# Optimization experiments

Measured on AMD Instinct MI355X. Metric: run time of the kernel, lower is better.

Reference implementation:

```python
import jax, jax.numpy as jnp
import numpy as np

N = 100000      # nodes
E = 1600000     # edges (avg degree 16)
IN = 128        # in_channels
OUT = 64        # out_channels
HID = 2 * OUT   # hidden = 2*out_channels


def setup_inputs() -> dict:
    key = jax.random.key(0)
    ks = jax.random.split(key, 9)
    x = jax.random.normal(ks[0], (N, IN), jnp.float32)
    edge_index = jax.random.randint(ks[1], (2, E), 0, N, jnp.int32)
    init_dist = jax.random.normal(ks[2], (N, OUT), jnp.float32)
    # GCNConv weights (glorot-ish scale) and biases
    W1 = jax.random.normal(ks[3], (IN, HID), jnp.float32) * (1.0 / np.sqrt(IN))
    b1 = jnp.zeros((HID,), jnp.float32)
    Wmu = jax.random.normal(ks[4], (HID, OUT), jnp.float32) * (1.0 / np.sqrt(HID))
    bmu = jnp.zeros((OUT,), jnp.float32)
    Wls = jax.random.normal(ks[5], (HID, OUT), jnp.float32) * (1.0 / np.sqrt(HID))
    bls = jnp.zeros((OUT,), jnp.float32)
    return {"x": x, "edge_index": edge_index, "init_dist": init_dist,
            "W1": W1, "b1": b1, "Wmu": Wmu, "bmu": bmu, "Wls": Wls, "bls": bls}


def _gcn(h, src, dst, norm, W, b, n):
    # dense transform, then normalized scatter-add aggregation over edges
    h = h @ W                               # [N, F]
    msg = h[src] * norm[:, None]            # gather + scale  [E', F]
    out = jax.ops.segment_sum(msg, dst, num_segments=n)
    return out + b


def reference(x, edge_index, init_dist, W1, b1, Wmu, bmu, Wls, bls):
    n = x.shape[0]
    # add self-loops (PyG GCNConv default)
    loops = jnp.arange(n, dtype=edge_index.dtype)
    src = jnp.concatenate([edge_index[0], loops])
    dst = jnp.concatenate([edge_index[1], loops])
    # symmetric normalization: deg over A+I, norm_e = d_src^-1/2 * d_dst^-1/2
    deg = jax.ops.segment_sum(jnp.ones_like(dst, dtype=x.dtype), dst, num_segments=n)
    dinv = jax.lax.rsqrt(jnp.maximum(deg, 1.0))  # deg >= 1 thanks to self-loops
    norm = dinv[src] * dinv[dst]

    h = _gcn(x, src, dst, norm, W1, b1, n)       # conv1 (no activation in source)
    mu = _gcn(h, src, dst, norm, Wmu, bmu, n)
    logstd = _gcn(h, src, dst, norm, Wls, bls, n)
    # reparametrize: mu + init_dist * exp(logstd)
    return mu + init_dist * jnp.exp(logstd)
```

## Files before the change

kernel.cpp:

```cpp
#include <hip/hip_runtime.h>
#include <hip/hip_bf16.h>
#include <math.h>

#define NN 100000
#define NE 1600000
#define SLOTS 48
#define NODES_PER_BUCKET 12500
#define SEGS 256
#define QUADS (NE / 4)
#define QPS ((QUADS + SEGS - 1) / SEGS)

__device__ __forceinline__ float bf2f(unsigned int u) {
    union { unsigned int u; float f; } c; c.u = u << 16; return c.f;
}
__device__ __forceinline__ unsigned short f2bf(float f) {
    union { float f; unsigned int u; } c; c.f = f;
    unsigned int x = c.u;
    return (unsigned short)((x + 0x7fffu + ((x >> 16) & 1u)) >> 16);
}

typedef __attribute__((ext_vector_type(8))) short short8;
typedef __attribute__((ext_vector_type(4))) float float4v;

__global__ __launch_bounds__(256) void k_count_fill_b(const int* __restrict__ ei,
        int* __restrict__ cnt, int* __restrict__ csr48) {
    int bucket = blockIdx.x & 7;
    int seg = blockIdx.x >> 3;
    int lo = bucket * NODES_PER_BUCKET, hi = lo + NODES_PER_BUCKET;
    int q1 = min((seg + 1) * QPS, QUADS);
    for (int q = seg * QPS + threadIdx.x; q < q1; q += 256) {
        int e0 = q * 4;
        int4 s = *(const int4*)(ei + e0);
        int4 d = *(const int4*)(ei + NE + e0);
        int r;
        if (d.x >= lo && d.x < hi) { r = atomicAdd(&cnt[d.x], 1); if (r < SLOTS) csr48[d.x * SLOTS + r] = s.x; }
        if (d.y >= lo && d.y < hi) { r = atomicAdd(&cnt[d.y], 1); if (r < SLOTS) csr48[d.y * SLOTS + r] = s.y; }
        if (d.z >= lo && d.z < hi) { r = atomicAdd(&cnt[d.z], 1); if (r < SLOTS) csr48[d.z * SLOTS + r] = s.z; }
        if (d.w >= lo && d.w < hi) { r = atomicAdd(&cnt[d.w], 1); if (r < SLOTS) csr48[d.w * SLOTS + r] = s.w; }
    }
}

__global__ __launch_bounds__(256) void k_prescale(const float* __restrict__ x,
        const int* __restrict__ cnt, float* __restrict__ dinv, unsigned short* __restrict__ xs) {
    int i = blockIdx.x * 256 + threadIdx.x;
    if (i >= NN * 32) return;
    int node = i >> 5, c = (i & 31) << 2;
    float d = rsqrtf((float)(cnt[node] + 1));
    if ((i & 31) == 0) dinv[node] = d;
    float4 v = *(const float4*)(x + (size_t)node * 128 + c);
    uint2 st;
    st.x = ((unsigned int)f2bf(d * v.y) << 16) | f2bf(d * v.x);
    st.y = ((unsigned int)f2bf(d * v.w) << 16) | f2bf(d * v.z);
    *(uint2*)(xs + (size_t)node * 128 + c) = st;
}

__global__ void k_wt(const float* __restrict__ W1, const float* __restrict__ Wmu,
                     const float* __restrict__ Wls,
                     unsigned short* __restrict__ W1t, unsigned short* __restrict__ W2t) {
    int idx = blockIdx.x * 256 + threadIdx.x;
    if (idx < 16384) {
        int n = idx >> 7, k = idx & 127;
        W1t[n * 128 + k] = f2bf(W1[k * 128 + n]);
    } else {
        int j = idx - 16384;
        int n = j >> 7, k = j & 127;
        float v = (n < 64) ? Wmu[k * 64 + n] : Wls[k * 64 + (n - 64)];
        W2t[n * 128 + k] = f2bf(v);
    }
}

__device__ __forceinline__ void gather_core(
    const unsigned short* __restrict__ tab,
    const int* __restrict__ csr, int base, int deg,
    int q, int l16, float* a) {
    int t = q;
    while (t + 4 < deg) {
        int s0 = csr[base + t];
        int s1 = csr[base + t + 4];
        uint4 r0 = *(const uint4*)(tab + (size_t)s0 * 128 + l16 * 8);
        uint4 r1 = *(const uint4*)(tab + (size_t)s1 * 128 + l16 * 8);
        a[0] += bf2f(r0.x & 0xffffu) + bf2f(r1.x & 0xffffu);
        a[1] += bf2f(r0.x >> 16)     + bf2f(r1.x >> 16);
        a[2] += bf2f(r0.y & 0xffffu) + bf2f(r1.y & 0xffffu);
        a[3] += bf2f(r0.y >> 16)     + bf2f(r1.y >> 16);
        a[4] += bf2f(r0.z & 0xffffu) + bf2f(r1.z & 0xffffu);
        a[5] += bf2f(r0.z >> 16)     + bf2f(r1.z >> 16);
        a[6] += bf2f(r0.w & 0xffffu) + bf2f(r1.w & 0xffffu);
        a[7] += bf2f(r0.w >> 16)     + bf2f(r1.w >> 16);
        t += 8;
    }
    while (t < deg) {
        int s = csr[base + t];
        uint4 r = *(const uint4*)(tab + (size_t)s * 128 + l16 * 8);
        a[0] += bf2f(r.x & 0xffffu); a[1] += bf2f(r.x >> 16);
        a[2] += bf2f(r.y & 0xffffu); a[3] += bf2f(r.y >> 16);
        a[4] += bf2f(r.z & 0xffffu); a[5] += bf2f(r.z >> 16);
        a[6] += bf2f(r.w & 0xffffu); a[7] += bf2f(r.w >> 16);
        t += 4;
    }
}

__global__ __launch_bounds__(256) void k_gatherA(
    const unsigned short* __restrict__ tab, const int* __restrict__ cnt,
    const int* __restrict__ csr48, const float* __restrict__ dinv,
    unsigned short* __restrict__ yout) {
    int node = blockIdx.x * 4 + (threadIdx.x >> 6);
    int lane = threadIdx.x & 63;
    int q = lane >> 4, l16 = lane & 15;
    float a[8] = {0.f, 0.f, 0.f, 0.f, 0.f, 0.f, 0.f, 0.f};
    if (q == 0) {
        uint4 p = *(const uint4*)(tab + (size_t)node * 128 + l16 * 8);
        a[0] = bf2f(p.x & 0xffffu); a[1] = bf2f(p.x >> 16);
        a[2] = bf2f(p.y & 0xffffu); a[3] = bf2f(p.y >> 16);
        a[4] = bf2f(p.z & 0xffffu); a[5] = bf2f(p.z >> 16);
        a[6] = bf2f(p.w & 0xffffu); a[7] = bf2f(p.w >> 16);
    }
    int deg = __builtin_amdgcn_readfirstlane(cnt[node]);
    if (deg > SLOTS) deg = SLOTS;
    gather_core(tab, csr48, node * SLOTS, deg, q, l16, a);
#pragma unroll
    for (int j = 0; j < 8; ++j) {
        a[j] += __shfl_xor(a[j], 16);
        a[j] += __shfl_xor(a[j], 32);
    }
    if (q == 0) {
        float di = dinv[node];
        uint4 st;
        st.x = ((unsigned int)f2bf(a[1] * di) << 16) | f2bf(a[0] * di);
        st.y = ((unsigned int)f2bf(a[3] * di) << 16) | f2bf(a[2] * di);
        st.z = ((unsigned int)f2bf(a[5] * di) << 16) | f2bf(a[4] * di);
        st.w = ((unsigned int)f2bf(a[7] * di) << 16) | f2bf(a[6] * di);
        *(uint4*)(yout + (size_t)node * 128 + l16 * 8) = st;
    }
}

__global__ __launch_bounds__(256) void k_gemm1(
    unsigned short* __restrict__ yio,
    const unsigned short* __restrict__ Bt,
    const float* __restrict__ bias,
    const float* __restrict__ dinv,
    int nrows) {
    __shared__ __align__(16) unsigned short As[64 * 136];
    int tid = threadIdx.x;
    int r0 = blockIdx.x * 64;
    for (int c = tid; c < 1024; c += 256) {
        int row = c >> 4, kc = (c & 15) << 3;
        int gr = r0 + row;
        short8 v = {0, 0, 0, 0, 0, 0, 0, 0};
        if (gr < nrows) v = *(const short8*)(yio + (size_t)gr * 128 + kc);
        *(short8*)(As + row * 136 + kc) = v;
    }
    __syncthreads();
    int lane = tid & 63, wave = tid >> 6;
    int quad = lane >> 4, l16 = lane & 15;
    int c0 = wave * 16 + l16;
    int c1 = 64 + c0;
    float4v acc[4][2];
#pragma unroll
    for (int rt = 0; rt < 4; ++rt) {
        float4v z = {0.f, 0.f, 0.f, 0.f};
        acc[rt][0] = z; acc[rt][1] = z;
    }
#pragma unroll
    for (int ks = 0; ks < 4; ++ks) {
        short8 b0 = *(const short8*)(Bt + (size_t)c0 * 128 + ks * 32 + quad * 8);
        short8 b1 = *(const short8*)(Bt + (size_t)c1 * 128 + ks * 32 + quad * 8);
        short8 af[4];
#pragma unroll
        for (int rt = 0; rt < 4; ++rt)
            af[rt] = *(const short8*)(As + (rt * 16 + l16) * 136 + ks * 32 + quad * 8);
#pragma unroll
        for (int rt = 0; rt < 4; ++rt) {
            acc[rt][0] = __builtin_amdgcn_mfma_f32_16x16x32_bf16(af[rt], b0, acc[rt][0], 0, 0, 0);
            acc[rt][1] = __builtin_amdgcn_mfma_f32_16x16x32_bf16(af[rt], b1, acc[rt][1], 0, 0, 0);
        }
    }
    float bc0 = bias[c0], bc1 = bias[c1];
#pragma unroll
    for (int rt = 0; rt < 4; ++rt)
#pragma unroll
        for (int reg = 0; reg < 4; ++reg) {
            int gr = r0 + rt * 16 + quad * 4 + reg;
            if (gr < nrows) {
                float dg = dinv[gr];
                yio[(size_t)gr * 128 + c0] = f2bf(dg * (acc[rt][0][reg] + bc0));
                yio[(size_t)gr * 128 + c1] = f2bf(dg * (acc[rt][1][reg] + bc1));
            }
        }
}

__global__ __launch_bounds__(256) void k_gemm2(
    const unsigned short* __restrict__ y2,
    const unsigned short* __restrict__ Bt,
    const float* __restrict__ bmu,
    const float* __restrict__ bls,
    const float* __restrict__ init,
    float* __restrict__ outp,
    int nrows) {
    __shared__ __align__(16) unsigned short As[64 * 136];
    int tid = threadIdx.x;
    int r0 = blockIdx.x * 64;
    for (int c = tid; c < 1024; c += 256) {
        int row = c >> 4, kc = (c & 15) << 3;
        int gr = r0 + row;
        short8 v = {0, 0, 0, 0, 0, 0, 0, 0};
        if (gr < nrows) v = *(const short8*)(y2 + (size_t)gr * 128 + kc);
        *(short8*)(As + row * 136 + kc) = v;
    }
    __syncthreads();
    int lane = tid & 63, wave = tid >> 6;
    int quad = lane >> 4, l16 = lane & 15;
    int cm = wave * 16 + l16;
    int cl = 64 + cm;
    float4v acc[4][2];
#pragma unroll
    for (int rt = 0; rt < 4; ++rt) {
        float4v z = {0.f, 0.f, 0.f, 0.f};
        acc[rt][0] = z; acc[rt][1] = z;
    }
#pragma unroll
    for (int ks = 0; ks < 4; ++ks) {
        short8 b0 = *(const short8*)(Bt + (size_t)cm * 128 + ks * 32 + quad * 8);
        short8 b1 = *(const short8*)(Bt + (size_t)cl * 128 + ks * 32 + quad * 8);
        short8 af[4];
#pragma unroll
        for (int rt = 0; rt < 4; ++rt)
            af[rt] = *(const short8*)(As + (rt * 16 + l16) * 136 + ks * 32 + quad * 8);
#pragma unroll
        for (int rt = 0; rt < 4; ++rt) {
            acc[rt][0] = __builtin_amdgcn_mfma_f32_16x16x32_bf16(af[rt], b0, acc[rt][0], 0, 0, 0);
            acc[rt][1] = __builtin_amdgcn_mfma_f32_16x16x32_bf16(af[rt], b1, acc[rt][1], 0, 0, 0);
        }
    }
    float bc_mu = bmu[cm], bc_ls = bls[cm];
#pragma unroll
    for (int rt = 0; rt < 4; ++rt)
#pragma unroll
        for (int reg = 0; reg < 4; ++reg) {
            int gr = r0 + rt * 16 + quad * 4 + reg;
            if (gr < nrows) {
                float mu = acc[rt][0][reg] + bc_mu;
                float ls = acc[rt][1][reg] + bc_ls;
                float idv = init[(size_t)gr * 64 + cm];
                outp[(size_t)gr * 64 + cm] = mu + idv * expf(ls);
            }
        }
}

extern "C" void kernel_launch(void* const* d_in, const int* in_sizes, int n_in,
                              void* d_out, int out_size, void* d_ws, size_t ws_size,
                              hipStream_t stream) {
    const float* x   = (const float*)d_in[0];
    const int*   ei  = (const int*)d_in[1];
    const float* ind = (const float*)d_in[2];
    const float* W1  = (const float*)d_in[3];
    const float* b1  = (const float*)d_in[4];
    const float* Wmu = (const float*)d_in[5];
    const float* bmu = (const float*)d_in[6];
    const float* Wls = (const float*)d_in[7];
    const float* bls = (const float*)d_in[8];
    float* outp = (float*)d_out;

    char* w = (char*)d_ws;
    auto carve = [&](size_t bytes) -> char* {
        char* p = w; w += (bytes + 255) & ~(size_t)255; return p;
    };
    int*   cnt  = (int*)carve((size_t)NN * 4);
    float* dinv = (float*)carve((size_t)NN * 4);
    unsigned short* W1t = (unsigned short*)carve(128 * 128 * 2);
    unsigned short* W2t = (unsigned short*)carve(128 * 128 * 2);
    unsigned short* xs  = (unsigned short*)carve((size_t)NN * 128 * 2);
    unsigned short* y   = (unsigned short*)carve((size_t)NN * 128 * 2);
    int* csr = (int*)carve((size_t)NN * SLOTS * 4);

    hipMemsetAsync(cnt, 0, (size_t)NN * 4, stream);
    k_wt<<<128, 256, 0, stream>>>(W1, Wmu, Wls, W1t, W2t);
    k_count_fill_b<<<8 * SEGS, 256, 0, stream>>>(ei, cnt, csr);
    k_prescale<<<(NN * 32 + 255) / 256, 256, 0, stream>>>(x, cnt, dinv, xs);
    k_gatherA<<<NN / 4, 256, 0, stream>>>(xs, cnt, csr, dinv, y);
    k_gemm1<<<(NN + 63) / 64, 256, 0, stream>>>(y, W1t, b1, dinv, NN);
    k_gatherA<<<NN / 4, 256, 0, stream>>>(y, cnt, csr, dinv, xs);
    k_gemm2<<<(NN + 63) / 64, 256, 0, stream>>>(xs, W2t, bmu, bls, ind, outp, NN);
}
```

Measured before the change: 386.8 us.

## Split feature tables into 16-column slabs and gather per slab for cache locality

Stores the intermediate bf16 node tables in a blocked layout of 8 column groups of 16 features (group-major), and rewrites the gather kernel so each block handles one column group for 32 nodes. A single group's slab is 3.2 MB, so random neighbor reads are meant to hit L2/MALL instead of spanning the full 25.6 MB table. The GEMM kernels and prescale are adapted to read and write the new layout. Nontemporal loads and stores are added for the edge list, CSR indices and gather outputs. The trade-off is that the CSR indices are now reread eight times, and each 32-byte row fetch is narrower.

Measured after the change: 618.1 us. 59.8% more time.

```diff
diff --git a/kernel.cpp b/kernel.cpp
--- a/kernel.cpp
+++ b/kernel.cpp
@@ -1,5 +1,4 @@
 #include <hip/hip_runtime.h>
-#include <hip/hip_bf16.h>
 #include <math.h>
 
 #define NN 100000
@@ -19,6 +18,8 @@
     return (unsigned short)((x + 0x7fffu + ((x >> 16) & 1u)) >> 16);
 }
 
+typedef __attribute__((ext_vector_type(4))) int int4v;
+typedef __attribute__((ext_vector_type(4))) unsigned int uint4v;
 typedef __attribute__((ext_vector_type(8))) short short8;
 typedef __attribute__((ext_vector_type(4))) float float4v;
 
@@ -28,15 +29,16 @@
     int seg = blockIdx.x >> 3;
     int lo = bucket * NODES_PER_BUCKET, hi = lo + NODES_PER_BUCKET;
     int q1 = min((seg + 1) * QPS, QUADS);
+    const int4v* eis = (const int4v*)ei;
+    const int4v* eid = (const int4v*)(ei + NE);
     for (int q = seg * QPS + threadIdx.x; q < q1; q += 256) {
-        int e0 = q * 4;
-        int4 s = *(const int4*)(ei + e0);
-        int4 d = *(const int4*)(ei + NE + e0);
+        int4v s = __builtin_nontemporal_load(eis + q);
+        int4v d = __builtin_nontemporal_load(eid + q);
         int r;
-        if (d.x >= lo && d.x < hi) { r = atomicAdd(&cnt[d.x], 1); if (r < SLOTS) csr48[d.x * SLOTS + r] = s.x; }
-        if (d.y >= lo && d.y < hi) { r = atomicAdd(&cnt[d.y], 1); if (r < SLOTS) csr48[d.y * SLOTS + r] = s.y; }
-        if (d.z >= lo && d.z < hi) { r = atomicAdd(&cnt[d.z], 1); if (r < SLOTS) csr48[d.z * SLOTS + r] = s.z; }
-        if (d.w >= lo && d.w < hi) { r = atomicAdd(&cnt[d.w], 1); if (r < SLOTS) csr48[d.w * SLOTS + r] = s.w; }
+        if (d[0] >= lo && d[0] < hi) { r = atomicAdd(&cnt[d[0]], 1); if (r < SLOTS) csr48[d[0] * SLOTS + r] = s[0]; }
+        if (d[1] >= lo && d[1] < hi) { r = atomicAdd(&cnt[d[1]], 1); if (r < SLOTS) csr48[d[1] * SLOTS + r] = s[1]; }
+        if (d[2] >= lo && d[2] < hi) { r = atomicAdd(&cnt[d[2]], 1); if (r < SLOTS) csr48[d[2] * SLOTS + r] = s[2]; }
+        if (d[3] >= lo && d[3] < hi) { r = atomicAdd(&cnt[d[3]], 1); if (r < SLOTS) csr48[d[3] * SLOTS + r] = s[3]; }
     }
 }
 
@@ -51,7 +53,8 @@
     uint2 st;
     st.x = ((unsigned int)f2bf(d * v.y) << 16) | f2bf(d * v.x);
     st.y = ((unsigned int)f2bf(d * v.w) << 16) | f2bf(d * v.z);
-    *(uint2*)(xs + (size_t)node * 128 + c) = st;
+    int g = c >> 4, off = c & 15;
+    *(uint2*)(xs + ((size_t)g * NN + node) * 16 + off) = st;
 }
 
 __global__ void k_wt(const float* __restrict__ W1, const float* __restrict__ Wmu,
@@ -69,68 +72,59 @@
     }
 }
 
-__device__ __forceinline__ void gather_core(
+__device__ __forceinline__ void acc8(const uint4v r, float* a) {
+    a[0] += bf2f(r[0] & 0xffffu); a[1] += bf2f(r[0] >> 16);
+    a[2] += bf2f(r[1] & 0xffffu); a[3] += bf2f(r[1] >> 16);
+    a[4] += bf2f(r[2] & 0xffffu); a[5] += bf2f(r[2] >> 16);
+    a[6] += bf2f(r[3] & 0xffffu); a[7] += bf2f(r[3] >> 16);
+}
+
+__global__ __launch_bounds__(256) void k_gatherB(
     const unsigned short* __restrict__ tab,
-    const int* __restrict__ csr, int base, int deg,
-    int q, int l16, float* a) {
-    int t = q;
-    while (t + 4 < deg) {
-        int s0 = csr[base + t];
-        int s1 = csr[base + t + 4];
-        uint4 r0 = *(const uint4*)(tab + (size_t)s0 * 128 + l16 * 8);
-        uint4 r1 = *(const uint4*)(tab + (size_t)s1 * 128 + l16 * 8);
-        a[0] += bf2f(r0.x & 0xffffu) + bf2f(r1.x & 0xffffu);
-        a[1] += bf2f(r0.x >> 16)     + bf2f(r1.x >> 16);
-        a[2] += bf2f(r0.y & 0xffffu) + bf2f(r1.y & 0xffffu);
-        a[3] += bf2f(r0.y >> 16)     + bf2f(r1.y >> 16);
-        a[4] += bf2f(r0.z & 0xffffu) + bf2f(r1.z & 0xffffu);
-        a[5] += bf2f(r0.z >> 16)     + bf2f(r1.z >> 16);
-        a[6] += bf2f(r0.w & 0xffffu) + bf2f(r1.w & 0xffffu);
-        a[7] += bf2f(r0.w >> 16)     + bf2f(r1.w >> 16);
-        t += 8;
-    }
-    while (t < deg) {
-        int s = csr[base + t];
-        uint4 r = *(const uint4*)(tab + (size_t)s * 128 + l16 * 8);
-        a[0] += bf2f(r.x & 0xffffu); a[1] += bf2f(r.x >> 16);
-        a[2] += bf2f(r.y & 0xffffu); a[3] += bf2f(r.y >> 16);
-        a[4] += bf2f(r.z & 0xffffu); a[5] += bf2f(r.z >> 16);
-        a[6] += bf2f(r.w & 0xffffu); a[7] += bf2f(r.w >> 16);
-        t += 4;
-    }
-}
-
-__global__ __launch_bounds__(256) void k_gatherA(
-    const unsigned short* __restrict__ tab, const int* __restrict__ cnt,
-    const int* __restrict__ csr48, const float* __restrict__ dinv,
+    const int* __restrict__ cnt,
+    const int* __restrict__ csr48,
+    const float* __restrict__ dinv,
     unsigned short* __restrict__ yout) {
-    int node = blockIdx.x * 4 + (threadIdx.x >> 6);
+    int g = blockIdx.x & 7;
+    int blk = blockIdx.x >> 3;
+    int wave = threadIdx.x >> 6;
     int lane = threadIdx.x & 63;
-    int q = lane >> 4, l16 = lane & 15;
-    float a[8] = {0.f, 0.f, 0.f, 0.f, 0.f, 0.f, 0.f, 0.f};
-    if (q == 0) {
-        uint4 p = *(const uint4*)(tab + (size_t)node * 128 + l16 * 8);
-        a[0] = bf2f(p.x & 0xffffu); a[1] = bf2f(p.x >> 16);
-        a[2] = bf2f(p.y & 0xffffu); a[3] = bf2f(p.y >> 16);
-        a[4] = bf2f(p.z & 0xffffu); a[5] = bf2f(p.z >> 16);
-        a[6] = bf2f(p.w & 0xffffu); a[7] = bf2f(p.w >> 16);
-    }
-    int deg = __builtin_amdgcn_readfirstlane(cnt[node]);
-    if (deg > SLOTS) deg = SLOTS;
-    gather_core(tab, csr48, node * SLOTS, deg, q, l16, a);
-#pragma unroll
-    for (int j = 0; j < 8; ++j) {
-        a[j] += __shfl_xor(a[j], 16);
-        a[j] += __shfl_xor(a[j], 32);
-    }
-    if (q == 0) {
-        float di = dinv[node];
-        uint4 st;
-        st.x = ((unsigned int)f2bf(a[1] * di) << 16) | f2bf(a[0] * di);
-        st.y = ((unsigned int)f2bf(a[3] * di) << 16) | f2bf(a[2] * di);
-        st.z = ((unsigned int)f2bf(a[5] * di) << 16) | f2bf(a[4] * di);
-        st.w = ((unsigned int)f2bf(a[7] * di) << 16) | f2bf(a[6] * di);
-        *(uint4*)(yout + (size_t)node * 128 + l16 * 8) = st;
+    int l = lane & 31;
+    int nsel = lane >> 5;
+    int slot = l >> 1, half = l & 1;
+    const unsigned short* tg = tab + (size_t)g * (NN * 16);
+    unsigned short* yg = yout + (size_t)g * (NN * 16);
+#pragma unroll 1
+    for (int it = 0; it < 4; ++it) {
+        int node = blk * 32 + it * 8 + wave * 2 + nsel;
+        float a[8] = {0.f, 0.f, 0.f, 0.f, 0.f, 0.f, 0.f, 0.f};
+        int deg = cnt[node]; if (deg > SLOTS) deg = SLOTS;
+        if (slot == 0) {
+            uint4v p = *(const uint4v*)(tg + (size_t)node * 16 + half * 8);
+            acc8(p, a);
+        }
+        int base = node * SLOTS;
+        for (int t = slot; t < deg; t += 16) {
+            int s = __builtin_nontemporal_load(csr48 + base + t);
+            uint4v r = *(const uint4v*)(tg + (size_t)s * 16 + half * 8);
+            acc8(r, a);
+        }
+#pragma unroll
+        for (int j = 0; j < 8; ++j) {
+            a[j] += __shfl_xor(a[j], 2);
+            a[j] += __shfl_xor(a[j], 4);
+            a[j] += __shfl_xor(a[j], 8);
+            a[j] += __shfl_xor(a[j], 16);
+        }
+        if (slot == 0) {
+            float di = dinv[node];
+            uint4v st;
+            st[0] = ((unsigned int)f2bf(a[1] * di) << 16) | f2bf(a[0] * di);
+            st[1] = ((unsigned int)f2bf(a[3] * di) << 16) | f2bf(a[2] * di);
+            st[2] = ((unsigned int)f2bf(a[5] * di) << 16) | f2bf(a[4] * di);
+            st[3] = ((unsigned int)f2bf(a[7] * di) << 16) | f2bf(a[6] * di);
+            __builtin_nontemporal_store(st, (uint4v*)(yg + (size_t)node * 16 + half * 8));
+        }
     }
 }
 
@@ -147,7 +141,8 @@
         int row = c >> 4, kc = (c & 15) << 3;
         int gr = r0 + row;
         short8 v = {0, 0, 0, 0, 0, 0, 0, 0};
-        if (gr < nrows) v = *(const short8*)(yio + (size_t)gr * 128 + kc);
+        if (gr < nrows)
+            v = *(const short8*)(yio + ((size_t)(kc >> 4) * NN + gr) * 16 + (kc & 15));
         *(short8*)(As + row * 136 + kc) = v;
     }
     __syncthreads();
@@ -176,6 +171,8 @@
         }
     }
     float bc0 = bias[c0], bc1 = bias[c1];
+    size_t g0 = (size_t)(c0 >> 4) * NN, g1 = (size_t)(c1 >> 4) * NN;
+    int o0 = c0 & 15, o1 = c1 & 15;
 #pragma unroll
     for (int rt = 0; rt < 4; ++rt)
 #pragma unroll
@@ -183,8 +180,8 @@
             int gr = r0 + rt * 16 + quad * 4 + reg;
             if (gr < nrows) {
                 float dg = dinv[gr];
-                yio[(size_t)gr * 128 + c0] = f2bf(dg * (acc[rt][0][reg] + bc0));
-                yio[(size_t)gr * 128 + c1] = f2bf(dg * (acc[rt][1][reg] + bc1));
+                yio[(g0 + gr) * 16 + o0] = f2bf(dg * (acc[rt][0][reg] + bc0));
+                yio[(g1 + gr) * 16 + o1] = f2bf(dg * (acc[rt][1][reg] + bc1));
             }
         }
 }
@@ -204,7 +201,8 @@
         int row = c >> 4, kc = (c & 15) << 3;
         int gr = r0 + row;
         short8 v = {0, 0, 0, 0, 0, 0, 0, 0};
-        if (gr < nrows) v = *(const short8*)(y2 + (size_t)gr * 128 + kc);
+        if (gr < nrows)
+            v = *(const short8*)(y2 + ((size_t)(kc >> 4) * NN + gr) * 16 + (kc & 15));
         *(short8*)(As + row * 136 + kc) = v;
     }
     __syncthreads();
@@ -277,8 +275,8 @@
     k_wt<<<128, 256, 0, stream>>>(W1, Wmu, Wls, W1t, W2t);
     k_count_fill_b<<<8 * SEGS, 256, 0, stream>>>(ei, cnt, csr);
     k_prescale<<<(NN * 32 + 255) / 256, 256, 0, stream>>>(x, cnt, dinv, xs);
-    k_gatherA<<<NN / 4, 256, 0, stream>>>(xs, cnt, csr, dinv, y);
+    k_gatherB<<<(NN / 32) * 8, 256, 0, stream>>>(xs, cnt, csr, dinv, y);
     k_gemm1<<<(NN + 63) / 64, 256, 0, stream>>>(y, W1t, b1, dinv, NN);
-    k_gatherA<<<NN / 4, 256, 0, stream>>>(y, cnt, csr, dinv, xs);
+    k_gatherB<<<(NN / 32) * 8, 256, 0, stream>>>(y, cnt, csr, dinv, xs);
     k_gemm2<<<(NN + 63) / 64, 256, 0, stream>>>(xs, W2t, bmu, bls, ind, outp, NN);
 }
```

## Bind CSR-build destination buckets to XCC with ticketed segments and sweep

Applied to the files above, without the earlier changes.

The CSR fill kernel now reads the hardware XCC ID and assigns each workgroup the destination-node bucket owned by its XCC. Segments are handed out dynamically through per-bucket atomic tickets. The per-node counter atomics use workgroup scope on the assumption that each bucket's counters are touched only by a single XCC's L2, and the edge reads are nontemporal. A follow-up single-block-per-bucket sweep kernel processes any segments left unclaimed, for example if some XCC got no blocks. This relies on undocumented XCC scheduling and relaxed atomic scope being coherent, and adds a serial tail kernel.

Measured after the change: 426.9 us. 1.1x slower.

```diff
diff --git a/kernel.cpp b/kernel.cpp
--- a/kernel.cpp
+++ b/kernel.cpp
@@ -1,5 +1,4 @@
 #include <hip/hip_runtime.h>
-#include <hip/hip_bf16.h>
 #include <math.h>
 
 #define NN 100000
@@ -19,24 +18,68 @@
     return (unsigned short)((x + 0x7fffu + ((x >> 16) & 1u)) >> 16);
 }
 
+typedef __attribute__((ext_vector_type(4))) int int4v;
 typedef __attribute__((ext_vector_type(8))) short short8;
 typedef __attribute__((ext_vector_type(4))) float float4v;
 
-__global__ __launch_bounds__(256) void k_count_fill_b(const int* __restrict__ ei,
-        int* __restrict__ cnt, int* __restrict__ csr48) {
-    int bucket = blockIdx.x & 7;
-    int seg = blockIdx.x >> 3;
+__global__ __launch_bounds__(256) void k_count_fill_x(const int* __restrict__ ei,
+        int* __restrict__ cnt, int* __restrict__ csr48, int* __restrict__ tickets) {
+    unsigned int xcc;
+    asm volatile("s_getreg_b32 %0, hwreg(HW_REG_XCC_ID)" : "=s"(xcc));
+    int bucket = (int)(xcc & 7u);
     int lo = bucket * NODES_PER_BUCKET, hi = lo + NODES_PER_BUCKET;
-    int q1 = min((seg + 1) * QPS, QUADS);
-    for (int q = seg * QPS + threadIdx.x; q < q1; q += 256) {
-        int e0 = q * 4;
-        int4 s = *(const int4*)(ei + e0);
-        int4 d = *(const int4*)(ei + NE + e0);
-        int r;
-        if (d.x >= lo && d.x < hi) { r = atomicAdd(&cnt[d.x], 1); if (r < SLOTS) csr48[d.x * SLOTS + r] = s.x; }
-        if (d.y >= lo && d.y < hi) { r = atomicAdd(&cnt[d.y], 1); if (r < SLOTS) csr48[d.y * SLOTS + r] = s.y; }
-        if (d.z >= lo && d.z < hi) { r = atomicAdd(&cnt[d.z], 1); if (r < SLOTS) csr48[d.z * SLOTS + r] = s.z; }
-        if (d.w >= lo && d.w < hi) { r = atomicAdd(&cnt[d.w], 1); if (r < SLOTS) csr48[d.w * SLOTS + r] = s.w; }
+    const int4v* eis = (const int4v*)ei;
+    const int4v* eid = (const int4v*)(ei + NE);
+    __shared__ int s_seg;
+    for (;;) {
+        __syncthreads();
+        if (threadIdx.x == 0) s_seg = atomicAdd(&tickets[bucket], 1);
+        __syncthreads();
+        int seg = s_seg;
+        if (seg >= SEGS) break;
+        int q1 = min((seg + 1) * QPS, QUADS);
+        for (int q = seg * QPS + (int)threadIdx.x; q < q1; q += 256) {
+            int4v s = __builtin_nontemporal_load(eis + q);
+            int4v d = __builtin_nontemporal_load(eid + q);
+#pragma unroll
+            for (int j = 0; j < 4; ++j) {
+                int dj = d[j];
+                if (dj >= lo && dj < hi) {
+                    int r = __hip_atomic_fetch_add(&cnt[dj], 1,
+                                __ATOMIC_RELAXED, __HIP_MEMORY_SCOPE_WORKGROUP);
+                    if (r < SLOTS) csr48[dj * SLOTS + r] = s[j];
+                }
+            }
+        }
+    }
+}
+
+__global__ __launch_bounds__(256) void k_sweep(const int* __restrict__ ei,
+        int* __restrict__ cnt, int* __restrict__ csr48, int* __restrict__ tickets) {
+    int bucket = blockIdx.x;
+    int lo = bucket * NODES_PER_BUCKET, hi = lo + NODES_PER_BUCKET;
+    const int4v* eis = (const int4v*)ei;
+    const int4v* eid = (const int4v*)(ei + NE);
+    __shared__ int s_seg;
+    for (;;) {
+        __syncthreads();
+        if (threadIdx.x == 0) s_seg = atomicAdd(&tickets[bucket], 1);
+        __syncthreads();
+        int seg = s_seg;
+        if (seg >= SEGS) break;
+        int q1 = min((seg + 1) * QPS, QUADS);
+        for (int q = seg * QPS + (int)threadIdx.x; q < q1; q += 256) {
+            int4v s = *(eis + q);
+            int4v d = *(eid + q);
+#pragma unroll
+            for (int j = 0; j < 4; ++j) {
+                int dj = d[j];
+                if (dj >= lo && dj < hi) {
+                    int r = atomicAdd(&cnt[dj], 1);
+                    if (r < SLOTS) csr48[dj * SLOTS + r] = s[j];
+                }
+            }
+        }
     }
 }
 
@@ -267,6 +310,7 @@
     };
     int*   cnt  = (int*)carve((size_t)NN * 4);
     float* dinv = (float*)carve((size_t)NN * 4);
+    int*   tickets = (int*)carve(8 * 4);
     unsigned short* W1t = (unsigned short*)carve(128 * 128 * 2);
     unsigned short* W2t = (unsigned short*)carve(128 * 128 * 2);
     unsigned short* xs  = (unsigned short*)carve((size_t)NN * 128 * 2);
@@ -274,8 +318,10 @@
     int* csr = (int*)carve((size_t)NN * SLOTS * 4);
 
     hipMemsetAsync(cnt, 0, (size_t)NN * 4, stream);
+    hipMemsetAsync(tickets, 0, 8 * 4, stream);
     k_wt<<<128, 256, 0, stream>>>(W1, Wmu, Wls, W1t, W2t);
-    k_count_fill_b<<<8 * SEGS, 256, 0, stream>>>(ei, cnt, csr);
+    k_count_fill_x<<<8 * SEGS, 256, 0, stream>>>(ei, cnt, csr, tickets);
+    k_sweep<<<8, 256, 0, stream>>>(ei, cnt, csr, tickets);
     k_prescale<<<(NN * 32 + 255) / 256, 256, 0, stream>>>(x, cnt, dinv, xs);
     k_gatherA<<<NN / 4, 256, 0, stream>>>(xs, cnt, csr, dinv, y);
     k_gemm1<<<(NN + 63) / 64, 256, 0, stream>>>(y, W1t, b1, dinv, NN);
```

## Fuse neighbor gather into GEMM kernels via LDS staging

Applied to the files above, without the earlier changes.

Merges each sparse aggregation kernel with the following dense MFMA GEMM. Each wave gathers 16 node rows directly into the shared-memory A tile instead of writing the aggregated bf16 rows to global memory and reading them back. This removes two kernel launches and a round trip of the intermediate through global memory. The trade-off is far fewer blocks (64 nodes per block instead of 4), so the latency-bound random gathers get less parallelism, and the MFMA work waits behind the slowest wave's gather.

Measured after the change: 462.9 us. 19.7% more time.

```diff
diff --git a/kernel.cpp b/kernel.cpp
--- a/kernel.cpp
+++ b/kernel.cpp
@@ -1,5 +1,4 @@
 #include <hip/hip_runtime.h>
-#include <hip/hip_bf16.h>
 #include <math.h>
 
 #define NN 100000
@@ -100,59 +99,60 @@
     }
 }
 
-__global__ __launch_bounds__(256) void k_gatherA(
+__device__ __forceinline__ void gather_node_to_lds(
     const unsigned short* __restrict__ tab, const int* __restrict__ cnt,
     const int* __restrict__ csr48, const float* __restrict__ dinv,
-    unsigned short* __restrict__ yout) {
-    int node = blockIdx.x * 4 + (threadIdx.x >> 6);
-    int lane = threadIdx.x & 63;
-    int q = lane >> 4, l16 = lane & 15;
+    unsigned short* __restrict__ As, int row, int node,
+    int q, int l16) {
     float a[8] = {0.f, 0.f, 0.f, 0.f, 0.f, 0.f, 0.f, 0.f};
+    bool ok = node < NN;
+    if (ok) {
+        if (q == 0) {
+            uint4 p = *(const uint4*)(tab + (size_t)node * 128 + l16 * 8);
+            a[0] = bf2f(p.x & 0xffffu); a[1] = bf2f(p.x >> 16);
+            a[2] = bf2f(p.y & 0xffffu); a[3] = bf2f(p.y >> 16);
+            a[4] = bf2f(p.z & 0xffffu); a[5] = bf2f(p.z >> 16);
+            a[6] = bf2f(p.w & 0xffffu); a[7] = bf2f(p.w >> 16);
+        }
+        int deg = __builtin_amdgcn_readfirstlane(cnt[node]);
+        if (deg > SLOTS) deg = SLOTS;
+        gather_core(tab, csr48, node * SLOTS, deg, q, l16, a);
+#pragma unroll
+        for (int j = 0; j < 8; ++j) {
+            a[j] += __shfl_xor(a[j], 16);
+            a[j] += __shfl_xor(a[j], 32);
+        }
+    }
     if (q == 0) {
-        uint4 p = *(const uint4*)(tab + (size_t)node * 128 + l16 * 8);
-        a[0] = bf2f(p.x & 0xffffu); a[1] = bf2f(p.x >> 16);
-        a[2] = bf2f(p.y & 0xffffu); a[3] = bf2f(p.y >> 16);
-        a[4] = bf2f(p.z & 0xffffu); a[5] = bf2f(p.z >> 16);
-        a[6] = bf2f(p.w & 0xffffu); a[7] = bf2f(p.w >> 16);
-    }
-    int deg = __builtin_amdgcn_readfirstlane(cnt[node]);
-    if (deg > SLOTS) deg = SLOTS;
-    gather_core(tab, csr48, node * SLOTS, deg, q, l16, a);
-#pragma unroll
-    for (int j = 0; j < 8; ++j) {
-        a[j] += __shfl_xor(a[j], 16);
-        a[j] += __shfl_xor(a[j], 32);
-    }
-    if (q == 0) {
-        float di = dinv[node];
+        float di = ok ? dinv[node] : 0.f;
         uint4 st;
         st.x = ((unsigned int)f2bf(a[1] * di) << 16) | f2bf(a[0] * di);
         st.y = ((unsigned int)f2bf(a[3] * di) << 16) | f2bf(a[2] * di);
         st.z = ((unsigned int)f2bf(a[5] * di) << 16) | f2bf(a[4] * di);
         st.w = ((unsigned int)f2bf(a[7] * di) << 16) | f2bf(a[6] * di);
-        *(uint4*)(yout + (size_t)node * 128 + l16 * 8) = st;
-    }
-}
-
-__global__ __launch_bounds__(256) void k_gemm1(
-    unsigned short* __restrict__ yio,
+        *(uint4*)(As + row * 136 + l16 * 8) = st;
+    }
+}
+
+__global__ __launch_bounds__(256) void k_fuse1(
+    const unsigned short* __restrict__ tab,
+    const int* __restrict__ cnt, const int* __restrict__ csr48,
+    const float* __restrict__ dinv,
     const unsigned short* __restrict__ Bt,
     const float* __restrict__ bias,
-    const float* __restrict__ dinv,
-    int nrows) {
+    unsigned short* __restrict__ yout) {
     __shared__ __align__(16) unsigned short As[64 * 136];
     int tid = threadIdx.x;
+    int lane = tid & 63, wave = tid >> 6;
+    int q = lane >> 4, l16 = lane & 15;
     int r0 = blockIdx.x * 64;
-    for (int c = tid; c < 1024; c += 256) {
-        int row = c >> 4, kc = (c & 15) << 3;
-        int gr = r0 + row;
-        short8 v = {0, 0, 0, 0, 0, 0, 0, 0};
-        if (gr < nrows) v = *(const short8*)(yio + (size_t)gr * 128 + kc);
-        *(short8*)(As + row * 136 + kc) = v;
+#pragma unroll 1
+    for (int rr = 0; rr < 16; ++rr) {
+        int row = wave * 16 + rr;
+        gather_node_to_lds(tab, cnt, csr48, dinv, As, row, r0 + row, q, l16);
     }
     __syncthreads();
-    int lane = tid & 63, wave = tid >> 6;
-    int quad = lane >> 4, l16 = lane & 15;
+    int quad = lane >> 4;
     int c0 = wave * 16 + l16;
     int c1 = 64 + c0;
     float4v acc[4][2];
@@ -181,35 +181,35 @@
 #pragma unroll
         for (int reg = 0; reg < 4; ++reg) {
             int gr = r0 + rt * 16 + quad * 4 + reg;
-            if (gr < nrows) {
+            if (gr < NN) {
                 float dg = dinv[gr];
-                yio[(size_t)gr * 128 + c0] = f2bf(dg * (acc[rt][0][reg] + bc0));
-                yio[(size_t)gr * 128 + c1] = f2bf(dg * (acc[rt][1][reg] + bc1));
+                yout[(size_t)gr * 128 + c0] = f2bf(dg * (acc[rt][0][reg] + bc0));
+                yout[(size_t)gr * 128 + c1] = f2bf(dg * (acc[rt][1][reg] + bc1));
             }
         }
 }
 
-__global__ __launch_bounds__(256) void k_gemm2(
-    const unsigned short* __restrict__ y2,
+__global__ __launch_bounds__(256) void k_fuse2(
+    const unsigned short* __restrict__ tab,
+    const int* __restrict__ cnt, const int* __restrict__ csr48,
+    const float* __restrict__ dinv,
     const unsigned short* __restrict__ Bt,
     const float* __restrict__ bmu,
     const float* __restrict__ bls,
     const float* __restrict__ init,
-    float* __restrict__ outp,
-    int nrows) {
+    float* __restrict__ outp) {
     __shared__ __align__(16) unsigned short As[64 * 136];
     int tid = threadIdx.x;
+    int lane = tid & 63, wave = tid >> 6;
+    int q = lane >> 4, l16 = lane & 15;
     int r0 = blockIdx.x * 64;
-    for (int c = tid; c < 1024; c += 256) {
-        int row = c >> 4, kc = (c & 15) << 3;
-        int gr = r0 + row;
-        short8 v = {0, 0, 0, 0, 0, 0, 0, 0};
-        if (gr < nrows) v = *(const short8*)(y2 + (size_t)gr * 128 + kc);
-        *(short8*)(As + row * 136 + kc) = v;
+#pragma unroll 1
+    for (int rr = 0; rr < 16; ++rr) {
+        int row = wave * 16 + rr;
+        gather_node_to_lds(tab, cnt, csr48, dinv, As, row, r0 + row, q, l16);
     }
     __syncthreads();
-    int lane = tid & 63, wave = tid >> 6;
-    int quad = lane >> 4, l16 = lane & 15;
+    int quad = lane >> 4;
     int cm = wave * 16 + l16;
     int cl = 64 + cm;
     float4v acc[4][2];
@@ -238,7 +238,7 @@
 #pragma unroll
         for (int reg = 0; reg < 4; ++reg) {
             int gr = r0 + rt * 16 + quad * 4 + reg;
-            if (gr < nrows) {
+            if (gr < NN) {
                 float mu = acc[rt][0][reg] + bc_mu;
                 float ls = acc[rt][1][reg] + bc_ls;
                 float idv = init[(size_t)gr * 64 + cm];
@@ -277,8 +277,6 @@
     k_wt<<<128, 256, 0, stream>>>(W1, Wmu, Wls, W1t, W2t);
     k_count_fill_b<<<8 * SEGS, 256, 0, stream>>>(ei, cnt, csr);
     k_prescale<<<(NN * 32 + 255) / 256, 256, 0, stream>>>(x, cnt, dinv, xs);
-    k_gatherA<<<NN / 4, 256, 0, stream>>>(xs, cnt, csr, dinv, y);
-    k_gemm1<<<(NN + 63) / 64, 256, 0, stream>>>(y, W1t, b1, dinv, NN);
-    k_gatherA<<<NN / 4, 256, 0, stream>>>(y, cnt, csr, dinv, xs);
-    k_gemm2<<<(NN + 63) / 64, 256, 0, stream>>>(xs, W2t, bmu, bls, ind, outp, NN);
-}
+    k_fuse1<<<(NN + 63) / 64, 256, 0, stream>>>(xs, cnt, csr, dinv, W1t, b1, y);
+    k_fuse2<<<(NN + 63) / 64, 256, 0, stream>>>(y, cnt, csr, dinv, W2t, bmu, bls, ind, outp);
+}
```
